# Kernel tuning notes

Measured on AMD Instinct MI355X. Metric: run time of the kernel, lower is better.

Reference implementation:

```python
import jax, jax.numpy as jnp
import numpy as np

H = 64  # hidden_size hardcoded in the module


def setup_inputs() -> dict:
    key = jax.random.key(0)
    ks = jax.random.split(key, 8)
    B, T, I, O = 4096, 256, 128, 10
    s_ih = 1.0 / np.sqrt(H)
    return {
        "x": jax.random.normal(ks[0], (B, T, I), dtype=jnp.float32),
        # PyTorch LSTM params, gate order (i, f, g, o)
        "W_ih": jax.random.uniform(ks[1], (4 * H, I), minval=-s_ih, maxval=s_ih, dtype=jnp.float32),
        "W_hh": jax.random.uniform(ks[2], (4 * H, H), minval=-s_ih, maxval=s_ih, dtype=jnp.float32),
        "b_ih": jax.random.uniform(ks[3], (4 * H,), minval=-s_ih, maxval=s_ih, dtype=jnp.float32),
        "b_hh": jax.random.uniform(ks[4], (4 * H,), minval=-s_ih, maxval=s_ih, dtype=jnp.float32),
        "W_out": jax.random.uniform(ks[5], (O, H), minval=-s_ih, maxval=s_ih, dtype=jnp.float32),
        "b_out": jax.random.uniform(ks[6], (O,), minval=-s_ih, maxval=s_ih, dtype=jnp.float32),
    }


def _lstm_last_h(x, W_ih, W_hh, b_ih, b_hh):
    B, T, I = x.shape
    # Precompute input contributions for all timesteps: [T, B, 4H]
    gx = jnp.einsum('bti,gi->tbg', x, W_ih) + (b_ih + b_hh)

    def step(carry, g_t):
        h, c = carry
        g = g_t + h @ W_hh.T  # [B, 4H]
        i = jax.nn.sigmoid(g[:, 0 * H:1 * H])
        f = jax.nn.sigmoid(g[:, 1 * H:2 * H])
        gg = jnp.tanh(g[:, 2 * H:3 * H])
        o = jax.nn.sigmoid(g[:, 3 * H:4 * H])
        c = f * c + i * gg
        h = o * jnp.tanh(c)
        return (h, c), None

    h0 = jnp.zeros((B, H), dtype=x.dtype)
    c0 = jnp.zeros((B, H), dtype=x.dtype)
    (h_last, _), _ = jax.lax.scan(step, (h0, c0), gx)
    return h_last


def reference(x, W_ih, W_hh, b_ih, b_hh, W_out, b_out):
    # forward reshapes x to [B, T, I]; our x is already that shape.
    h_last = _lstm_last_h(x, W_ih, W_hh, b_ih, b_hh)  # r_out[:, -1, :]
    return h_last @ W_out.T + b_out
```

## Files before the change

### kernel.cpp

```cpp
#include <hip/hip_runtime.h>


typedef __attribute__((ext_vector_type(8))) short bf16x8;
typedef __attribute__((ext_vector_type(4))) float f32x4;
typedef __attribute__((ext_vector_type(2))) unsigned u32x2;

#define T_STEPS 256
#define L2E 1.44269504f

#define XF_OFF 0
#define HA_OFF 16384
#define HB_OFF 18432
#define HF_OFF 20480
#define LDS_SZ 22528

__device__ __forceinline__ short f2bf(float f) {
    unsigned u = __float_as_uint(f);
    u += 0x7FFFu + ((u >> 16) & 1u);
    return (short)(u >> 16);
}
__device__ __forceinline__ unsigned cvt_pk(float lo, float hi) {
    unsigned r;
    asm("v_cvt_pk_bf16_f32 %0, %1, %2" : "=v"(r) : "v"(lo), "v"(hi));
    return r;
}
__device__ __forceinline__ float frcp(float x) { float r; asm("v_rcp_f32 %0, %1" : "=v"(r) : "v"(x)); return r; }
__device__ __forceinline__ float fexp2_raw(float x) { float r; asm("v_exp_f32 %0, %1" : "=v"(r) : "v"(x)); return r; }
__device__ __forceinline__ float fexp2c(float x) {
    return fexp2_raw(fminf(fmaxf(x, -40.0f), 40.0f));
}

#define MF(A, Bf, C) (C) = __builtin_amdgcn_mfma_f32_16x16x32_bf16((A), (Bf), (C), 0, 0, 0)
#define SYNC __syncthreads();

__global__ __launch_bounds__(256, 2) void lstm_kernel(
    const float* __restrict__ x,
    const float* __restrict__ W_ih,
    const float* __restrict__ W_hh,
    const float* __restrict__ b_ih,
    const float* __restrict__ b_hh,
    const float* __restrict__ W_out,
    const float* __restrict__ b_out,
    float* __restrict__ out)
{
    __shared__ __align__(16) char smem[LDS_SZ];

    const int tid  = threadIdx.x;
    const int lane = tid & 63;
    const int q    = tid >> 6;
    const int l15  = lane & 15;
    const int l4   = lane >> 4;
    const int b0   = blockIdx.x * 8;

    {
        const f32x4 z = (f32x4){0.f, 0.f, 0.f, 0.f};
        for (int i = tid; i < LDS_SZ / 16; i += 256)
            ((f32x4*)smem)[i] = z;
    }
    SYNC;

    bf16x8 Bih[4][4];
    bf16x8 Bhh[4][2];
    f32x4  biasC[4];
#pragma unroll
    for (int nt = 0; nt < 4; ++nt) {
        const float scl = (nt == 2) ? (2.0f * L2E) : (-L2E);
        const int row = nt * 64 + q * 16 + l15;
#pragma unroll
        for (int ks = 0; ks < 4; ++ks) {
            const float* p = W_ih + row * 128 + ks * 32 + l4 * 8;
            f32x4 a = *(const f32x4*)p;
            f32x4 b = *(const f32x4*)(p + 4);
            bf16x8 wv;
#pragma unroll
            for (int j = 0; j < 4; ++j) { wv[j] = f2bf(a[j] * scl); wv[4 + j] = f2bf(b[j] * scl); }
            Bih[nt][ks] = wv;
        }
#pragma unroll
        for (int ks = 0; ks < 2; ++ks) {
            const float* p = W_hh + row * 64 + ks * 32 + l4 * 8;
            f32x4 a = *(const f32x4*)p;
            f32x4 b = *(const f32x4*)(p + 4);
            bf16x8 wv;
#pragma unroll
            for (int j = 0; j < 4; ++j) { wv[j] = f2bf(a[j] * scl); wv[4 + j] = f2bf(b[j] * scl); }
            Bhh[nt][ks] = wv;
        }
        const float bb = (b_ih[row] + b_hh[row]) * scl;
        biasC[nt] = (f32x4){bb, bb, bb, bb};
    }

    int xf_rd[4];
#pragma unroll
    for (int ks = 0; ks < 4; ++ks)
        xf_rd[ks] = (((ks * 64 + lane) * 16) ^ ((ks & 3) << 6));

    const int jcol = q * 16 + l15;
    int hbA_wr[2], hbB_wr[2];
#pragma unroll
    for (int u = 0; u < 2; ++u) {
        const int trA = l4 * 4 + u;
        const int trB = trA + 2;
        hbA_wr[u] = ((trA * 128 + jcol * 2) ^ ((trA & 7) << 4) ^ ((trA >> 3) << 5));
        hbB_wr[u] = ((trB * 128 + jcol * 2) ^ ((trB & 7) << 4) ^ ((trB >> 3) << 5));
    }
    int hb_rd[2];
#pragma unroll
    for (int ks = 0; ks < 2; ++ks)
        hb_rd[ks] = ((l15 * 128 + ks * 64 + l4 * 16) ^ ((l15 & 7) << 4) ^ ((l15 >> 3) << 5));

    const int v   = tid >> 5;
    const int scc = tid & 31;
    const int sks = scc >> 3;
    const int sl4 = (scc & 7) >> 1;
    const int sh  = scc & 1;
    const int tr0 = 4 * (v >> 1) + (v & 1);
    const int bs  = 2 * (v >> 1) + (v & 1);
    const int xf_wr0 = (((sks * 64 + sl4 * 16 + tr0) * 16 + sh * 8) ^ ((sks & 3) << 6));
    const int xf_wr1 = (((sks * 64 + sl4 * 16 + tr0 + 2) * 16 + sh * 8) ^ ((sks & 3) << 6));
    const float* xsrc = x + (size_t)(b0 + bs) * (T_STEPS * 128) + scc * 4;

#pragma unroll
    for (int s = 0; s < 2; ++s) {
        f32x4 ve = *(const f32x4*)(xsrc + (size_t)(2 * s) * 128);
        f32x4 vo = *(const f32x4*)(xsrc + (size_t)(2 * s + 1) * 128);
        u32x2 we; we.x = cvt_pk(ve[0], ve[1]); we.y = cvt_pk(ve[2], ve[3]);
        u32x2 wo; wo.x = cvt_pk(vo[0], vo[1]); wo.y = cvt_pk(vo[2], vo[3]);
        *(u32x2*)(smem + XF_OFF + s * 4096 + xf_wr0) = we;
        *(u32x2*)(smem + XF_OFF + s * 4096 + xf_wr1) = wo;
    }
    f32x4 P0 = *(const f32x4*)(xsrc + 4 * 128);
    f32x4 P1 = *(const f32x4*)(xsrc + 5 * 128);

    SYNC;

    float c[2]  = {0.f, 0.f};
    float hl[2] = {0.f, 0.f};

    f32x4 accA[4], accB[4];

#define XGEMM(ACC, XPTR)                                                       \
    {                                                                          \
        bf16x8 Ax0 = *(const bf16x8*)((XPTR) + xf_rd[0]);                      \
        bf16x8 Ax1 = *(const bf16x8*)((XPTR) + xf_rd[1]);                      \
        bf16x8 Ax2 = *(const bf16x8*)((XPTR) + xf_rd[2]);                      \
        bf16x8 Ax3 = *(const bf16x8*)((XPTR) + xf_rd[3]);                      \
        ACC[0] = biasC[0]; ACC[1] = biasC[1];                                  \
        ACC[2] = biasC[2]; ACC[3] = biasC[3];                                  \
        MF(Ax0, Bih[0][0], ACC[0]); MF(Ax0, Bih[1][0], ACC[1]);                \
        MF(Ax0, Bih[2][0], ACC[2]); MF(Ax0, Bih[3][0], ACC[3]);                \
        MF(Ax1, Bih[0][1], ACC[0]); MF(Ax1, Bih[1][1], ACC[1]);                \
        MF(Ax1, Bih[2][1], ACC[2]); MF(Ax1, Bih[3][1], ACC[3]);                \
        MF(Ax2, Bih[0][2], ACC[0]); MF(Ax2, Bih[1][2], ACC[1]);                \
        MF(Ax2, Bih[2][2], ACC[2]); MF(Ax2, Bih[3][2], ACC[3]);                \
        MF(Ax3, Bih[0][3], ACC[0]); MF(Ax3, Bih[1][3], ACC[1]);                \
        MF(Ax3, Bih[2][3], ACC[2]); MF(Ax3, Bih[3][3], ACC[3]);                \
    }

    XGEMM(accA, smem + XF_OFF);

#define ALGEBRA(EI, EF, EG, EO, U)                                             \
    {                                                                          \
      float u_  = 1.0f + (EI);                                                 \
      float v_  = (EG) + 1.0f;                                                 \
      float w_  = 1.0f + (EF);                                                 \
      float uv_ = u_ * v_;                                                     \
      float num = __builtin_fmaf(c[U], uv_, ((EG) - 1.0f) * w_);               \
      c[U] = fminf(fmaxf(num * frcp(uv_ * w_), -30.0f), 30.0f);                \
      float E2_ = fexp2c(c[U] * (2.0f * L2E));                                 \
      hl[U] = (E2_ - 1.0f) * frcp((E2_ + 1.0f) * (1.0f + (EO)));               \
    }

#define WINDOW(W, ACUR, ANXT)                                                  \
  {                                                                            \
    const char* xrd = smem + XF_OFF + ((((W) + 1) & 3) * 4096);                \
    char*       xwr = smem + XF_OFF + ((((W) + 2) & 3) * 4096);                \
    char* hA = smem + HA_OFF;                                                  \
    char* hB = smem + HB_OFF;                                                  \
    bf16x8 Ah0 = *(const bf16x8*)(hA + hb_rd[0]);                              \
    bf16x8 Ah1 = *(const bf16x8*)(hA + hb_rd[1]);                              \
    MF(Ah0, Bhh[0][0], ACUR[0]); MF(Ah0, Bhh[1][0], ACUR[1]);                  \
    MF(Ah0, Bhh[2][0], ACUR[2]); MF(Ah0, Bhh[3][0], ACUR[3]);                  \
    MF(Ah1, Bhh[0][1], ACUR[0]); MF(Ah1, Bhh[1][1], ACUR[1]);                  \
    MF(Ah1, Bhh[2][1], ACUR[2]); MF(Ah1, Bhh[3][1], ACUR[3]);                  \
    float Ei0 = fexp2c(ACUR[0][0]), Ei1 = fexp2c(ACUR[0][1]);                  \
    float Ef0 = fexp2c(ACUR[1][0]), Ef1 = fexp2c(ACUR[1][1]);                  \
    float Eg0 = fexp2c(ACUR[2][0]), Eg1 = fexp2c(ACUR[2][1]);                  \
    float Eo0 = fexp2c(ACUR[3][0]), Eo1 = fexp2c(ACUR[3][1]);                  \
    XGEMM(ANXT, xrd);                                      \
    ALGEBRA(Ei0, Ef0, Eg0, Eo0, 0)                                             \
    ALGEBRA(Ei1, Ef1, Eg1, Eo1, 1)                                             \
    {                                                                          \
      unsigned wp = cvt_pk(hl[0], hl[1]);                                      \
      *(short*)(hB + hbB_wr[0]) = (short)wp;                                   \
      *(short*)(hB + hbB_wr[1]) = (short)(wp >> 16);                           \
    }                                                                          \
    SYNC;                                                                      \
    bf16x8 Bh0 = *(const bf16x8*)(hB + hb_rd[0]);                              \
    bf16x8 Bh1 = *(const bf16x8*)(hB + hb_rd[1]);                              \
    MF(Bh0, Bhh[0][0], ACUR[0]); MF(Bh0, Bhh[1][0], ACUR[1]);                  \
    MF(Bh0, Bhh[2][0], ACUR[2]); MF(Bh0, Bhh[3][0], ACUR[3]);                  \
    MF(Bh1, Bhh[0][1], ACUR[0]); MF(Bh1, Bhh[1][1], ACUR[1]);                  \
    MF(Bh1, Bhh[2][1], ACUR[2]); MF(Bh1, Bhh[3][1], ACUR[3]);                  \
    float Fi0 = fexp2c(ACUR[0][2]), Fi1 = fexp2c(ACUR[0][3]);                  \
    float Ff0 = fexp2c(ACUR[1][2]), Ff1 = fexp2c(ACUR[1][3]);                  \
    float Fg0 = fexp2c(ACUR[2][2]), Fg1 = fexp2c(ACUR[2][3]);                  \
    float Fo0 = fexp2c(ACUR[3][2]), Fo1 = fexp2c(ACUR[3][3]);                  \
    {                                                                          \
      u32x2 wv0; wv0.x = cvt_pk(P0[0], P0[1]); wv0.y = cvt_pk(P0[2], P0[3]);   \
      u32x2 wv1; wv1.x = cvt_pk(P1[0], P1[1]); wv1.y = cvt_pk(P1[2], P1[3]);   \
      *(u32x2*)(xwr + xf_wr0) = wv0;                                           \
      *(u32x2*)(xwr + xf_wr1) = wv1;                                           \
      const int tc = (2 * ((W) + 3)) & 255;                                    \
      P0 = *(const f32x4*)(xsrc + (size_t)tc * 128);                           \
      P1 = *(const f32x4*)(xsrc + (size_t)(tc + 1) * 128);                     \
    }                                                                          \
    ALGEBRA(Fi0, Ff0, Fg0, Fo0, 0)                                             \
    ALGEBRA(Fi1, Ff1, Fg1, Fo1, 1)                                             \
    {                                                                          \
      unsigned wp = cvt_pk(hl[0], hl[1]);                                      \
      *(short*)(hA + hbA_wr[0]) = (short)wp;                                   \
      *(short*)(hA + hbA_wr[1]) = (short)(wp >> 16);                           \
    }                                                                          \
    SYNC;                                                                      \
  }

    for (int w = 0; w < 128; w += 2) {
        WINDOW(w,     accA, accB);
        WINDOW(w + 1, accB, accA);
    }
#undef WINDOW
#undef XGEMM
#undef ALGEBRA

#pragma unroll
    for (int u = 0; u < 2; ++u) {
        const int b = 2 * l4 + u;
        *(float*)(smem + HF_OFF + (b * 64 + jcol) * 4) = hl[u];
    }
    SYNC;

    if (tid < 80) {
        const int b = tid / 10;
        const int o = tid - b * 10;
        const f32x4* hf = (const f32x4*)(smem + HF_OFF + b * 256);
        const f32x4* wr = (const f32x4*)(W_out + o * 64);
        float s = b_out[o];
#pragma unroll
        for (int j4 = 0; j4 < 16; ++j4) {
            f32x4 h4 = hf[j4];
            f32x4 w4 = wr[j4];
            s += h4[0] * w4[0] + h4[1] * w4[1] + h4[2] * w4[2] + h4[3] * w4[3];
        }
        out[(b0 + b) * 10 + o] = s;
    }
}

extern "C" void kernel_launch(void* const* d_in, const int* in_sizes, int n_in,
                              void* d_out, int out_size, void* d_ws, size_t ws_size,
                              hipStream_t stream) {
    const float* x     = (const float*)d_in[0];
    const float* W_ih  = (const float*)d_in[1];
    const float* W_hh  = (const float*)d_in[2];
    const float* b_ih  = (const float*)d_in[3];
    const float* b_hh  = (const float*)d_in[4];
    const float* W_out = (const float*)d_in[5];
    const float* b_out = (const float*)d_in[6];
    (void)in_sizes; (void)n_in; (void)out_size; (void)d_ws; (void)ws_size;

    lstm_kernel<<<dim3(512), dim3(256), 0, stream>>>(
        x, W_ih, W_hh, b_ih, b_hh, W_out, b_out, (float*)d_out);
}
```

Before: 182.0 us.

## Load x fragments straight into registers instead of staging through LDS

Each lane now loads its MFMA A-fragment of x directly from global memory into 8 float4 registers, one timestep window ahead, and packs it to bf16 in registers. This removes the 16KB LDS ring buffer for x, its swizzled writes and reads, and the cooperative staging loads. LDS per block drops to 6KB and the initial zeroing loop shrinks. In exchange, global loads become less coalesced (each lane reads scattered 32-byte pieces), register pressure rises, and only one window of prefetch covers global latency.

```diff
diff --git a/kernel.cpp b/kernel.cpp
--- a/kernel.cpp
+++ b/kernel.cpp
@@ -3,16 +3,14 @@
 
 typedef __attribute__((ext_vector_type(8))) short bf16x8;
 typedef __attribute__((ext_vector_type(4))) float f32x4;
-typedef __attribute__((ext_vector_type(2))) unsigned u32x2;
 
 #define T_STEPS 256
 #define L2E 1.44269504f
 
-#define XF_OFF 0
-#define HA_OFF 16384
-#define HB_OFF 18432
-#define HF_OFF 20480
-#define LDS_SZ 22528
+#define HA_OFF 0
+#define HB_OFF 2048
+#define HF_OFF 4096
+#define LDS_SZ 6144
 
 __device__ __forceinline__ short f2bf(float f) {
     unsigned u = __float_as_uint(f);
@@ -28,6 +26,12 @@
 __device__ __forceinline__ float fexp2_raw(float x) { float r; asm("v_exp_f32 %0, %1" : "=v"(r) : "v"(x)); return r; }
 __device__ __forceinline__ float fexp2c(float x) {
     return fexp2_raw(fminf(fmaxf(x, -40.0f), 40.0f));
+}
+__device__ __forceinline__ bf16x8 packfrag(f32x4 a, f32x4 b) {
+    union { bf16x8 s; unsigned u[4]; } w;
+    w.u[0] = cvt_pk(a[0], a[1]); w.u[1] = cvt_pk(a[2], a[3]);
+    w.u[2] = cvt_pk(b[0], b[1]); w.u[3] = cvt_pk(b[2], b[3]);
+    return w.s;
 }
 
 #define MF(A, Bf, C) (C) = __builtin_amdgcn_mfma_f32_16x16x32_bf16((A), (Bf), (C), 0, 0, 0)
@@ -52,12 +56,7 @@
     const int l4   = lane >> 4;
     const int b0   = blockIdx.x * 8;
 
-    {
-        const f32x4 z = (f32x4){0.f, 0.f, 0.f, 0.f};
-        for (int i = tid; i < LDS_SZ / 16; i += 256)
-            ((f32x4*)smem)[i] = z;
-    }
-    SYNC;
+    ((f32x4*)smem)[tid] = (f32x4){0.f, 0.f, 0.f, 0.f};
 
     bf16x8 Bih[4][4];
     bf16x8 Bhh[4][2];
@@ -90,11 +89,6 @@
         biasC[nt] = (f32x4){bb, bb, bb, bb};
     }
 
-    int xf_rd[4];
-#pragma unroll
-    for (int ks = 0; ks < 4; ++ks)
-        xf_rd[ks] = (((ks * 64 + lane) * 16) ^ ((ks & 3) << 6));
-
     const int jcol = q * 16 + l15;
     int hbA_wr[2], hbB_wr[2];
 #pragma unroll
@@ -109,55 +103,48 @@
     for (int ks = 0; ks < 2; ++ks)
         hb_rd[ks] = ((l15 * 128 + ks * 64 + l4 * 16) ^ ((l15 & 7) << 4) ^ ((l15 >> 3) << 5));
 
-    const int v   = tid >> 5;
-    const int scc = tid & 31;
-    const int sks = scc >> 3;
-    const int sl4 = (scc & 7) >> 1;
-    const int sh  = scc & 1;
-    const int tr0 = 4 * (v >> 1) + (v & 1);
-    const int bs  = 2 * (v >> 1) + (v & 1);
-    const int xf_wr0 = (((sks * 64 + sl4 * 16 + tr0) * 16 + sh * 8) ^ ((sks & 3) << 6));
-    const int xf_wr1 = (((sks * 64 + sl4 * 16 + tr0 + 2) * 16 + sh * 8) ^ ((sks & 3) << 6));
-    const float* xsrc = x + (size_t)(b0 + bs) * (T_STEPS * 128) + scc * 4;
-
-#pragma unroll
-    for (int s = 0; s < 2; ++s) {
-        f32x4 ve = *(const f32x4*)(xsrc + (size_t)(2 * s) * 128);
-        f32x4 vo = *(const f32x4*)(xsrc + (size_t)(2 * s + 1) * 128);
-        u32x2 we; we.x = cvt_pk(ve[0], ve[1]); we.y = cvt_pk(ve[2], ve[3]);
-        u32x2 wo; wo.x = cvt_pk(vo[0], vo[1]); wo.y = cvt_pk(vo[2], vo[3]);
-        *(u32x2*)(smem + XF_OFF + s * 4096 + xf_wr0) = we;
-        *(u32x2*)(smem + XF_OFF + s * 4096 + xf_wr1) = wo;
-    }
-    f32x4 P0 = *(const f32x4*)(xsrc + 4 * 128);
-    f32x4 P1 = *(const f32x4*)(xsrc + 5 * 128);
-
-    SYNC;
+    const int bb = 2 * (l15 >> 2) + (l15 & 1);
+    const int pp = (l15 >> 1) & 1;
+    const float* xlane = x + (size_t)(b0 + bb) * (T_STEPS * 128) + l4 * 8;
+
+    f32x4 XR[8];
+#define XLOAD(TE)                                                              \
+    {                                                                          \
+      int t_ = (TE) + pp; t_ = t_ > 255 ? 255 : t_;                            \
+      const float* s_ = xlane + (size_t)t_ * 128;                              \
+      XR[0] = *(const f32x4*)(s_);       XR[1] = *(const f32x4*)(s_ + 4);      \
+      XR[2] = *(const f32x4*)(s_ + 32);  XR[3] = *(const f32x4*)(s_ + 36);     \
+      XR[4] = *(const f32x4*)(s_ + 64);  XR[5] = *(const f32x4*)(s_ + 68);     \
+      XR[6] = *(const f32x4*)(s_ + 96);  XR[7] = *(const f32x4*)(s_ + 100);    \
+    }
+
+#define XGEMM_R(ACC)                                                           \
+    {                                                                          \
+        bf16x8 G0 = packfrag(XR[0], XR[1]);                                    \
+        bf16x8 G1 = packfrag(XR[2], XR[3]);                                    \
+        bf16x8 G2 = packfrag(XR[4], XR[5]);                                    \
+        bf16x8 G3 = packfrag(XR[6], XR[7]);                                    \
+        ACC[0] = biasC[0]; ACC[1] = biasC[1];                                  \
+        ACC[2] = biasC[2]; ACC[3] = biasC[3];                                  \
+        MF(G0, Bih[0][0], ACC[0]); MF(G0, Bih[1][0], ACC[1]);                  \
+        MF(G0, Bih[2][0], ACC[2]); MF(G0, Bih[3][0], ACC[3]);                  \
+        MF(G1, Bih[0][1], ACC[0]); MF(G1, Bih[1][1], ACC[1]);                  \
+        MF(G1, Bih[2][1], ACC[2]); MF(G1, Bih[3][1], ACC[3]);                  \
+        MF(G2, Bih[0][2], ACC[0]); MF(G2, Bih[1][2], ACC[1]);                  \
+        MF(G2, Bih[2][2], ACC[2]); MF(G2, Bih[3][2], ACC[3]);                  \
+        MF(G3, Bih[0][3], ACC[0]); MF(G3, Bih[1][3], ACC[1]);                  \
+        MF(G3, Bih[2][3], ACC[2]); MF(G3, Bih[3][3], ACC[3]);                  \
+    }
 
     float c[2]  = {0.f, 0.f};
     float hl[2] = {0.f, 0.f};
-
     f32x4 accA[4], accB[4];
 
-#define XGEMM(ACC, XPTR)                                                       \
-    {                                                                          \
-        bf16x8 Ax0 = *(const bf16x8*)((XPTR) + xf_rd[0]);                      \
-        bf16x8 Ax1 = *(const bf16x8*)((XPTR) + xf_rd[1]);                      \
-        bf16x8 Ax2 = *(const bf16x8*)((XPTR) + xf_rd[2]);                      \
-        bf16x8 Ax3 = *(const bf16x8*)((XPTR) + xf_rd[3]);                      \
-        ACC[0] = biasC[0]; ACC[1] = biasC[1];                                  \
-        ACC[2] = biasC[2]; ACC[3] = biasC[3];                                  \
-        MF(Ax0, Bih[0][0], ACC[0]); MF(Ax0, Bih[1][0], ACC[1]);                \
-        MF(Ax0, Bih[2][0], ACC[2]); MF(Ax0, Bih[3][0], ACC[3]);                \
-        MF(Ax1, Bih[0][1], ACC[0]); MF(Ax1, Bih[1][1], ACC[1]);                \
-        MF(Ax1, Bih[2][1], ACC[2]); MF(Ax1, Bih[3][1], ACC[3]);                \
-        MF(Ax2, Bih[0][2], ACC[0]); MF(Ax2, Bih[1][2], ACC[1]);                \
-        MF(Ax2, Bih[2][2], ACC[2]); MF(Ax2, Bih[3][2], ACC[3]);                \
-        MF(Ax3, Bih[0][3], ACC[0]); MF(Ax3, Bih[1][3], ACC[1]);                \
-        MF(Ax3, Bih[2][3], ACC[2]); MF(Ax3, Bih[3][3], ACC[3]);                \
-    }
-
-    XGEMM(accA, smem + XF_OFF);
+    XLOAD(0);
+    XGEMM_R(accA);
+    XLOAD(2);
+
+    SYNC;
 
 #define ALGEBRA(EI, EF, EG, EO, U)                                             \
     {                                                                          \
@@ -173,8 +160,6 @@
 
 #define WINDOW(W, ACUR, ANXT)                                                  \
   {                                                                            \
-    const char* xrd = smem + XF_OFF + ((((W) + 1) & 3) * 4096);                \
-    char*       xwr = smem + XF_OFF + ((((W) + 2) & 3) * 4096);                \
     char* hA = smem + HA_OFF;                                                  \
     char* hB = smem + HB_OFF;                                                  \
     bf16x8 Ah0 = *(const bf16x8*)(hA + hb_rd[0]);                              \
@@ -187,7 +172,7 @@
     float Ef0 = fexp2c(ACUR[1][0]), Ef1 = fexp2c(ACUR[1][1]);                  \
     float Eg0 = fexp2c(ACUR[2][0]), Eg1 = fexp2c(ACUR[2][1]);                  \
     float Eo0 = fexp2c(ACUR[3][0]), Eo1 = fexp2c(ACUR[3][1]);                  \
-    XGEMM(ANXT, xrd);                                      \
+    XGEMM_R(ANXT);                            \
     ALGEBRA(Ei0, Ef0, Eg0, Eo0, 0)                                             \
     ALGEBRA(Ei1, Ef1, Eg1, Eo1, 1)                                             \
     {                                                                          \
@@ -196,6 +181,7 @@
       *(short*)(hB + hbB_wr[1]) = (short)(wp >> 16);                           \
     }                                                                          \
     SYNC;                                                                      \
+    XLOAD(2 * (W) + 4);                    \
     bf16x8 Bh0 = *(const bf16x8*)(hB + hb_rd[0]);                              \
     bf16x8 Bh1 = *(const bf16x8*)(hB + hb_rd[1]);                              \
     MF(Bh0, Bhh[0][0], ACUR[0]); MF(Bh0, Bhh[1][0], ACUR[1]);                  \
@@ -206,15 +192,6 @@
     float Ff0 = fexp2c(ACUR[1][2]), Ff1 = fexp2c(ACUR[1][3]);                  \
     float Fg0 = fexp2c(ACUR[2][2]), Fg1 = fexp2c(ACUR[2][3]);                  \
     float Fo0 = fexp2c(ACUR[3][2]), Fo1 = fexp2c(ACUR[3][3]);                  \
-    {                                                                          \
-      u32x2 wv0; wv0.x = cvt_pk(P0[0], P0[1]); wv0.y = cvt_pk(P0[2], P0[3]);   \
-      u32x2 wv1; wv1.x = cvt_pk(P1[0], P1[1]); wv1.y = cvt_pk(P1[2], P1[3]);   \
-      *(u32x2*)(xwr + xf_wr0) = wv0;                                           \
-      *(u32x2*)(xwr + xf_wr1) = wv1;                                           \
-      const int tc = (2 * ((W) + 3)) & 255;                                    \
-      P0 = *(const f32x4*)(xsrc + (size_t)tc * 128);                           \
-      P1 = *(const f32x4*)(xsrc + (size_t)(tc + 1) * 128);                     \
-    }                                                                          \
     ALGEBRA(Fi0, Ff0, Fg0, Fo0, 0)                                             \
     ALGEBRA(Fi1, Ff1, Fg1, Fo1, 1)                                             \
     {                                                                          \
@@ -230,7 +207,8 @@
         WINDOW(w + 1, accB, accA);
     }
 #undef WINDOW
-#undef XGEMM
+#undef XGEMM_R
+#undef XLOAD
 #undef ALGEBRA
 
 #pragma unroll
```

Result: slower. 288.8 us (+58.7%).
